# Kernel optimization log

Hardware: AMD Instinct MI355X
Metric: run time of the kernel (lower is better)

Reference implementation:

```python
import jax, jax.numpy as jnp
import numpy as np

N = 4096   # query tokens
M = 4096   # key/value tokens
D = 512    # embedding_dim


def setup_inputs() -> dict:
    key = jax.random.key(0)
    kq, kk, kv = jax.random.split(key, 3)
    return {
        "query": jax.random.normal(kq, (N, D), dtype=jnp.float32),
        "key": jax.random.normal(kk, (M, D), dtype=jnp.float32),
        "value": jax.random.normal(kv, (M, D), dtype=jnp.float32),
    }


def reference(query, key, value):
    # scores = Q K^T  (no 1/sqrt(d) scaling in the original module)
    attention_scores = jnp.einsum("nd,md->nm", query, key)  # [N, M]
    attention_probs = jax.nn.softmax(attention_scores, axis=-1)  # [N, M]
    output = jnp.einsum("nm,md->nd", attention_probs, value)  # [N, D]
    return (output, attention_probs)
```

## Files before the change

kernel.cpp:

```cpp
#include <hip/hip_runtime.h>
#include <hip/hip_bf16.h>
#include <stdint.h>

#define N_Q 4096
#define N_K 4096
#define DIM 512

typedef float f32x4 __attribute__((ext_vector_type(4)));
typedef __bf16 bf16x8 __attribute__((ext_vector_type(8)));
typedef unsigned short u16x4 __attribute__((ext_vector_type(4)));
typedef int i32x4 __attribute__((ext_vector_type(4)));

__device__ __forceinline__ f32x4 mfma_bf16(bf16x8 a, bf16x8 b, f32x4 c) {
  return __builtin_amdgcn_mfma_f32_16x16x32_bf16(a, b, c, 0, 0, 0);
}

__device__ __forceinline__ i32x4 mfma_i8(i32x4 a, i32x4 b, i32x4 c) {
  return __builtin_amdgcn_mfma_i32_16x16x64_i8(a, b, c, 0, 0, 0);
}

__device__ __forceinline__ void gload16(const void* g, void* l) {
  __builtin_amdgcn_global_load_lds((const __attribute__((address_space(1))) void*)g,
                                   (__attribute__((address_space(3))) void*)l,
                                   16, 0, 0);
}

__device__ __forceinline__ void split4(const f32x4 v, u16x4& h, u16x4& l) {
#pragma unroll
  for (int i = 0; i < 4; ++i) {
    float f = v[i];
    uint32_t u = __builtin_bit_cast(uint32_t, f);
    uint32_t hb = (u + 0x8000u) & 0xffff0000u;
    float hf = __builtin_bit_cast(float, hb);
    float lf = f - hf;
    h[i] = (unsigned short)(hb >> 16);
    l[i] = (unsigned short)(__builtin_bit_cast(uint32_t, lf) >> 16);
  }
}

__device__ __forceinline__ unsigned short bf16r(float f) {
  uint32_t u = __builtin_bit_cast(uint32_t, f);
  return (unsigned short)((u + 0x8000u) >> 16);
}

__global__ __launch_bounds__(256) void quant_kernel(const float* __restrict__ Q,
                                                    const float* __restrict__ K,
                                                    signed char* __restrict__ Xq8,
                                                    signed char* __restrict__ Xk8,
                                                    float* __restrict__ sclA,
                                                    float* __restrict__ sclB) {
  const float* X = blockIdx.y ? K : Q;
  signed char* X8 = blockIdx.y ? Xk8 : Xq8;
  float* scl = blockIdx.y ? sclB : sclA;

  const int lane = threadIdx.x & 63;
  const int row = blockIdx.x * 4 + (threadIdx.x >> 6);

  f32x4 v[2];
  v[0] = *(const f32x4*)(X + (size_t)row * DIM + lane * 8);
  v[1] = *(const f32x4*)(X + (size_t)row * DIM + lane * 8 + 4);

  float mx = 0.f;
#pragma unroll
  for (int u = 0; u < 2; ++u)
#pragma unroll
    for (int j = 0; j < 4; ++j) mx = fmaxf(mx, fabsf(v[u][j]));
#pragma unroll
  for (int o = 32; o > 0; o >>= 1) mx = fmaxf(mx, __shfl_xor(mx, o, 64));

  const float s = fmaxf(mx, 1e-20f) * (1.0f / 127.0f);
  const float rinv = 1.0f / s;
  const float linv = 128.0f * rinv;

  uint32_t hw[2], lw[2];
#pragma unroll
  for (int u = 0; u < 2; ++u) {
    uint32_t hword = 0, lword = 0;
#pragma unroll
    for (int j = 0; j < 4; ++j) {
      float x = v[u][j];
      int h = __float2int_rn(x * rinv);
      float r = x - s * (float)h;
      int l = __float2int_rn(r * linv);
      hword |= ((uint32_t)(h & 0xff)) << (8 * j);
      lword |= ((uint32_t)(l & 0xff)) << (8 * j);
    }
    hw[u] = hword; lw[u] = lword;
  }
  uint2 hv; hv.x = hw[0]; hv.y = hw[1];
  uint2 lv; lv.x = lw[0]; lv.y = lw[1];
  *(uint2*)(X8 + (size_t)row * 1024 + lane * 8) = hv;
  *(uint2*)(X8 + (size_t)row * 1024 + 512 + lane * 8) = lv;
  if (lane == 0) scl[row] = s;
}

__global__ __launch_bounds__(256, 2) void qk4_kernel(const signed char* __restrict__ Xq8,
                                                     const signed char* __restrict__ Xk8,
                                                     const float* __restrict__ sclA,
                                                     const float* __restrict__ sclB,
                                                     float* __restrict__ S) {
  __shared__ __align__(16) char smem[65536];

  const int tid = threadIdx.x;
  const int lane = tid & 63, wid = tid >> 6;
  const int wr = wid >> 1, wc = wid & 1;

  const int bid = blockIdx.x;
  const int b = (bid & 7) * 128 + (bid >> 3);
  const int rbase = (b >> 5) * 128;
  const int cbase = (b & 31) * 128;

  const int lrow = lane >> 3;
  const int lchk = lane & 7;

  const i32x4 izero = {0, 0, 0, 0};
  i32x4 acc_hh[4][4], acc_x[4][4];
#pragma unroll
  for (int m = 0; m < 4; ++m)
#pragma unroll
    for (int n = 0; n < 4; ++n) { acc_hh[m][n] = izero; acc_x[m][n] = izero; }

  auto stage = [&](int buf, int t) {
#pragma unroll
    for (int i = 0; i < 4; ++i) {
      const int r = (wid << 5) + (i << 3) + lrow;
      const int sc = lchk ^ (r & 7);
      const int colb = (sc < 4) ? (t * 64 + sc * 16) : (512 + t * 64 + (sc & 3) * 16);
      const signed char* g = Xq8 + (size_t)(rbase + r) * 1024 + colb;
      uint32_t off = (uint32_t)(buf * 32768 + (((wid << 5) + (i << 3)) << 7));
      off = (uint32_t)__builtin_amdgcn_readfirstlane((int)off);
      gload16(g, smem + off);
    }
#pragma unroll
    for (int i = 0; i < 4; ++i) {
      const int r = (wid << 5) + (i << 3) + lrow;
      const int sc = lchk ^ (r & 7);
      const int colb = (sc < 4) ? (t * 64 + sc * 16) : (512 + t * 64 + (sc & 3) * 16);
      const signed char* g = Xk8 + (size_t)(cbase + r) * 1024 + colb;
      uint32_t off = (uint32_t)(buf * 32768 + 16384 + (((wid << 5) + (i << 3)) << 7));
      off = (uint32_t)__builtin_amdgcn_readfirstlane((int)off);
      gload16(g, smem + off);
    }
  };

  auto compute = [&](int buf) {
    const char* bA = smem + buf * 32768;
    const char* bB = bA + 16384;
    const int kc = lane >> 4;
    i32x4 ah[4], al[4], bh[4], bl[4];
#pragma unroll
    for (int m = 0; m < 4; ++m) {
      int row = (wr << 6) + (m << 4) + (lane & 15);
      ah[m] = *(const i32x4*)(bA + row * 128 + ((kc ^ (row & 7)) << 4));
      al[m] = *(const i32x4*)(bA + row * 128 + (((4 + kc) ^ (row & 7)) << 4));
    }
#pragma unroll
    for (int n = 0; n < 4; ++n) {
      int row = (wc << 6) + (n << 4) + (lane & 15);
      bh[n] = *(const i32x4*)(bB + row * 128 + ((kc ^ (row & 7)) << 4));
      bl[n] = *(const i32x4*)(bB + row * 128 + (((4 + kc) ^ (row & 7)) << 4));
    }
    __builtin_amdgcn_s_setprio(1);
#pragma unroll
    for (int m = 0; m < 4; ++m)
#pragma unroll
      for (int n = 0; n < 4; ++n) {
        acc_hh[m][n] = mfma_i8(ah[m], bh[n], acc_hh[m][n]);
        acc_x[m][n]  = mfma_i8(ah[m], bl[n], acc_x[m][n]);
        acc_x[m][n]  = mfma_i8(al[m], bh[n], acc_x[m][n]);
      }
    __builtin_amdgcn_s_setprio(0);
  };

  stage(0, 0);
  stage(1, 1);
  for (int t = 0; t < 8; ++t) {
    if (t < 7) asm volatile("s_waitcnt vmcnt(8)" ::: "memory");
    else       asm volatile("s_waitcnt vmcnt(0)" ::: "memory");
    __builtin_amdgcn_s_barrier();
    compute(t & 1);
    asm volatile("s_waitcnt lgkmcnt(0)" ::: "memory");
    __builtin_amdgcn_sched_barrier(0);
    __builtin_amdgcn_s_barrier();
    if (t + 2 < 8) stage(t & 1, t + 2);
  }

#pragma unroll
  for (int m = 0; m < 4; ++m) {
    int row0 = rbase + wr * 64 + m * 16 + (lane >> 4) * 4;
    float sa[4];
#pragma unroll
    for (int j = 0; j < 4; ++j) sa[j] = sclA[row0 + j];
#pragma unroll
    for (int n = 0; n < 4; ++n) {
      int col = cbase + wc * 64 + n * 16 + (lane & 15);
      float sb = sclB[col];
#pragma unroll
      for (int j = 0; j < 4; ++j) {
        float f = (float)acc_hh[m][n][j] + (float)acc_x[m][n][j] * 0.0078125f;
        S[(size_t)(row0 + j) * N_K + col] = sa[j] * sb * f;
      }
    }
  }
}

__global__ __launch_bounds__(256, 2) void qk_kernel(const float* __restrict__ Q,
                                                    const float* __restrict__ K,
                                                    float* __restrict__ S) {
  __shared__ __align__(16) char sAh[16384];
  __shared__ __align__(16) char sAl[16384];
  __shared__ __align__(16) char sBh[16384];
  __shared__ __align__(16) char sBl[16384];

  const int tid = threadIdx.x;
  const int rbase = blockIdx.y * 128;
  const int cbase = blockIdx.x * 128;
  const int lane = tid & 63, wid = tid >> 6;
  const int wr = wid >> 1, wc = wid & 1;
  const int lr = lane & 15, lk = (lane >> 4) * 8;

  const int srow = tid >> 4;
  const int scol = (tid & 15) * 4;

  f32x4 qr[8], kr[8];
#pragma unroll
  for (int p = 0; p < 8; ++p) {
    int r = p * 16 + srow;
    qr[p] = *(const f32x4*)(Q + (size_t)(rbase + r) * DIM + scol);
    kr[p] = *(const f32x4*)(K + (size_t)(cbase + r) * DIM + scol);
  }

  const f32x4 fzero = {0.f, 0.f, 0.f, 0.f};
  f32x4 acc[4][4];
#pragma unroll
  for (int m = 0; m < 4; ++m)
#pragma unroll
    for (int n = 0; n < 4; ++n) acc[m][n] = fzero;

  for (int kk = 0; kk < DIM / 64; ++kk) {
    __syncthreads();
#pragma unroll
    for (int p = 0; p < 8; ++p) {
      int r = p * 16 + srow;
      uint32_t bo = (uint32_t)(r * 128) + (uint32_t)((scol * 2) ^ ((r & 7) << 4));
      u16x4 qh, ql, kh, kl;
      split4(qr[p], qh, ql);
      split4(kr[p], kh, kl);
      *(u16x4*)(sAh + bo) = qh;
      *(u16x4*)(sAl + bo) = ql;
      *(u16x4*)(sBh + bo) = kh;
      *(u16x4*)(sBl + bo) = kl;
    }
    __syncthreads();
    if (kk < DIM / 64 - 1) {
#pragma unroll
      for (int p = 0; p < 8; ++p) {
        int r = p * 16 + srow;
        qr[p] = *(const f32x4*)(Q + (size_t)(rbase + r) * DIM + (kk + 1) * 64 + scol);
        kr[p] = *(const f32x4*)(K + (size_t)(cbase + r) * DIM + (kk + 1) * 64 + scol);
      }
    }
#pragma unroll
    for (int kh = 0; kh < 2; ++kh) {
      bf16x8 a_h[4], a_l[4], b_h[4], b_l[4];
#pragma unroll
      for (int m = 0; m < 4; ++m) {
        int row = wr * 64 + m * 16 + lr;
        uint32_t co = (uint32_t)(((kh * 32 + lk) * 2) ^ ((row & 7) << 4));
        a_h[m] = *(const bf16x8*)(sAh + row * 128 + co);
        a_l[m] = *(const bf16x8*)(sAl + row * 128 + co);
      }
#pragma unroll
      for (int n = 0; n < 4; ++n) {
        int row = wc * 64 + n * 16 + lr;
        uint32_t co = (uint32_t)(((kh * 32 + lk) * 2) ^ ((row & 7) << 4));
        b_h[n] = *(const bf16x8*)(sBh + row * 128 + co);
        b_l[n] = *(const bf16x8*)(sBl + row * 128 + co);
      }
#pragma unroll
      for (int m = 0; m < 4; ++m)
#pragma unroll
        for (int n = 0; n < 4; ++n) {
          acc[m][n] = mfma_bf16(a_h[m], b_h[n], acc[m][n]);
          acc[m][n] = mfma_bf16(a_h[m], b_l[n], acc[m][n]);
          acc[m][n] = mfma_bf16(a_l[m], b_h[n], acc[m][n]);
        }
    }
  }

#pragma unroll
  for (int m = 0; m < 4; ++m) {
    int row = rbase + wr * 64 + m * 16 + (lane >> 4) * 4;
#pragma unroll
    for (int n = 0; n < 4; ++n) {
      int col = cbase + wc * 64 + n * 16 + lr;
#pragma unroll
      for (int j = 0; j < 4; ++j)
        S[(size_t)(row + j) * N_K + col] = acc[m][n][j];
    }
  }
}

__global__ __launch_bounds__(256) void softmax_kernel(float* __restrict__ P,
                                                      unsigned short* __restrict__ Pb) {
  const int tid = threadIdx.x;
  const int wid = tid >> 6, lane = tid & 63;
  float* p = P + (size_t)blockIdx.x * N_K;

  f32x4 v[4];
  float mx = -3.0e38f;
#pragma unroll
  for (int i = 0; i < 4; ++i) {
    v[i] = *(const f32x4*)(p + i * 1024 + tid * 4);
    mx = fmaxf(mx, fmaxf(fmaxf(v[i][0], v[i][1]), fmaxf(v[i][2], v[i][3])));
  }
#pragma unroll
  for (int o = 32; o > 0; o >>= 1) mx = fmaxf(mx, __shfl_xor(mx, o, 64));
  __shared__ float redM[4];
  __shared__ float redS[4];
  if (lane == 0) redM[wid] = mx;
  __syncthreads();
  mx = fmaxf(fmaxf(redM[0], redM[1]), fmaxf(redM[2], redM[3]));

  float s = 0.f;
#pragma unroll
  for (int i = 0; i < 4; ++i) {
#pragma unroll
    for (int j = 0; j < 4; ++j) {
      v[i][j] = __expf(v[i][j] - mx);
      s += v[i][j];
    }
  }
#pragma unroll
  for (int o = 32; o > 0; o >>= 1) s += __shfl_xor(s, o, 64);
  if (lane == 0) redS[wid] = s;
  __syncthreads();
  s = redS[0] + redS[1] + redS[2] + redS[3];
  const float inv = 1.0f / s;

  unsigned short* pb = Pb ? (Pb + (size_t)blockIdx.x * N_K) : nullptr;
#pragma unroll
  for (int i = 0; i < 4; ++i) {
    v[i] *= inv;
    *(f32x4*)(p + i * 1024 + tid * 4) = v[i];
    if (pb) {
      u16x4 h;
#pragma unroll
      for (int j = 0; j < 4; ++j) h[j] = bf16r(v[i][j]);
      *(u16x4*)(pb + i * 1024 + tid * 4) = h;
    }
  }
}

__global__ __launch_bounds__(256) void vt_kernel(const float* __restrict__ V,
                                                 unsigned short* __restrict__ Vt) {
  __shared__ unsigned short t[64][72];
  const int tid = threadIdx.x;
  const int d0 = blockIdx.x * 64;
  const int k0 = blockIdx.y * 64;

#pragma unroll
  for (int c = 0; c < 4; ++c) {
    int kr = (tid >> 4) + c * 16;
    f32x4 v = *(const f32x4*)(V + (size_t)(k0 + kr) * DIM + d0 + (tid & 15) * 4);
#pragma unroll
    for (int j = 0; j < 4; ++j) t[(tid & 15) * 4 + j][kr] = bf16r(v[j]);
  }
  __syncthreads();
#pragma unroll
  for (int c = 0; c < 2; ++c) {
    int d = (tid >> 3) + c * 32;
    int k = (tid & 7) * 8;
    *(uint4*)(Vt + (size_t)(d0 + d) * N_K + k0 + k) = *(const uint4*)&t[d][k];
  }
}

__global__ __launch_bounds__(256) void zero_kernel(float* __restrict__ O) {
  const f32x4 z = {0.f, 0.f, 0.f, 0.f};
  *(f32x4*)(O + ((size_t)blockIdx.x * 256 + threadIdx.x) * 4) = z;
}

__global__ __launch_bounds__(256, 2) void pv4_kernel(const unsigned short* __restrict__ Pb,
                                                     const unsigned short* __restrict__ Vt,
                                                     float* __restrict__ O) {
  __shared__ __align__(16) char smem[65536];

  const int tid = threadIdx.x;
  const int lane = tid & 63, wid = tid >> 6;
  const int wr = wid >> 1, wc = wid & 1;
  const int rbase = blockIdx.y * 128;
  const int cbase = blockIdx.x * 128;
  const int k0 = blockIdx.z * 1024;

  const int lrow = lane >> 3;
  const int lchk = lane & 7;

  const f32x4 fzero = {0.f, 0.f, 0.f, 0.f};
  f32x4 acc[4][4];
#pragma unroll
  for (int m = 0; m < 4; ++m)
#pragma unroll
    for (int n = 0; n < 4; ++n) acc[m][n] = fzero;

  auto stage = [&](int buf, int t) {
    const size_t kel = (size_t)k0 + ((size_t)t << 6);
#pragma unroll
    for (int i = 0; i < 4; ++i) {
      const int rr = (wid << 5) + (i << 3) + lrow;
      const int gc = lchk ^ (rr & 7);
      const void* gA = (const void*)(Pb + (size_t)(rbase + rr) * N_K + kel + (gc << 3));
      uint32_t off = (uint32_t)(buf * 32768 + (((wid << 5) + (i << 3)) << 7));
      off = (uint32_t)__builtin_amdgcn_readfirstlane((int)off);
      gload16(gA, smem + off);
    }
#pragma unroll
    for (int i = 0; i < 4; ++i) {
      const int rr = (wid << 5) + (i << 3) + lrow;
      const int gc = lchk ^ (rr & 7);
      const void* gB = (const void*)(Vt + (size_t)(cbase + rr) * N_K + kel + (gc << 3));
      uint32_t off = (uint32_t)(buf * 32768 + 16384 + (((wid << 5) + (i << 3)) << 7));
      off = (uint32_t)__builtin_amdgcn_readfirstlane((int)off);
      gload16(gB, smem + off);
    }
  };

  auto compute = [&](int buf) {
    const char* bA = smem + buf * 32768;
    const char* bB = bA + 16384;
#pragma unroll
    for (int kh = 0; kh < 2; ++kh) {
      bf16x8 a[4], bfr[4];
#pragma unroll
      for (int m = 0; m < 4; ++m) {
        int row = (wr << 6) + (m << 4) + (lane & 15);
        uint32_t co = (uint32_t)(((((kh << 2) + (lane >> 4)) << 4)) ^ ((row & 7) << 4));
        a[m] = *(const bf16x8*)(bA + row * 128 + co);
      }
#pragma unroll
      for (int n = 0; n < 4; ++n) {
        int row = (wc << 6) + (n << 4) + (lane & 15);
        uint32_t co = (uint32_t)(((((kh << 2) + (lane >> 4)) << 4)) ^ ((row & 7) << 4));
        bfr[n] = *(const bf16x8*)(bB + row * 128 + co);
      }
      __builtin_amdgcn_s_setprio(1);
#pragma unroll
      for (int m = 0; m < 4; ++m)
#pragma unroll
        for (int n = 0; n < 4; ++n)
          acc[m][n] = mfma_bf16(a[m], bfr[n], acc[m][n]);
      __builtin_amdgcn_s_setprio(0);
    }
  };

  stage(0, 0);
  stage(1, 1);
  for (int t = 0; t < 16; ++t) {
    if (t < 15) asm volatile("s_waitcnt vmcnt(8)" ::: "memory");
    else        asm volatile("s_waitcnt vmcnt(0)" ::: "memory");
    __builtin_amdgcn_s_barrier();
    compute(t & 1);
    asm volatile("s_waitcnt lgkmcnt(0)" ::: "memory");
    __builtin_amdgcn_sched_barrier(0);
    __builtin_amdgcn_s_barrier();
    if (t + 2 < 16) stage(t & 1, t + 2);
  }

#pragma unroll
  for (int m = 0; m < 4; ++m) {
    int row = rbase + wr * 64 + m * 16 + (lane >> 4) * 4;
#pragma unroll
    for (int n = 0; n < 4; ++n) {
      int col = cbase + wc * 64 + n * 16 + (lane & 15);
#pragma unroll
      for (int j = 0; j < 4; ++j)
        atomicAdd(&O[(size_t)(row + j) * DIM + col], acc[m][n][j]);
    }
  }
}

__global__ __launch_bounds__(512, 2) void pv_kernel(const float* __restrict__ P,
                                                    const float* __restrict__ V,
                                                    float* __restrict__ O) {
  __shared__ __align__(16) char sA[16384];
  __shared__ __align__(16) char sB[16384];

  const int tid = threadIdx.x;
  const int rbase = blockIdx.y * 128;
  const int cbase = blockIdx.x * 128;
  const int lane = tid & 63, wid = tid >> 6;
  const int wr = wid >> 2, wc = wid & 3;
  const int lr = lane & 15, lk = (lane >> 4) * 8;

  const int a_row = tid >> 4;
  const int a_col = (tid & 15) * 4;
  const int b_c = tid & 127;
  const int b_oct = tid >> 7;

  f32x4 areg[4];
  float breg[4][4];
#pragma unroll
  for (int p = 0; p < 4; ++p) {
    int r = p * 32 + a_row;
    areg[p] = *(const f32x4*)(P + (size_t)(rbase + r) * N_K + a_col);
  }
#pragma unroll
  for (int g = 0; g < 4; ++g) {
    int kr0 = b_oct * 4 + g * 16;
#pragma unroll
    for (int i = 0; i < 4; ++i)
      breg[g][i] = V[(size_t)(kr0 + i) * DIM + cbase + b_c];
  }

  const f32x4 fzero = {0.f, 0.f, 0.f, 0.f};
  f32x4 acc[4][2];
#pragma unroll
  for (int m = 0; m < 4; ++m)
#pragma unroll
    for (int n = 0; n < 2; ++n) acc[m][n] = fzero;

  for (int kk = 0; kk < N_K / 64; ++kk) {
    __syncthreads();
#pragma unroll
    for (int p = 0; p < 4; ++p) {
      int r = p * 32 + a_row;
      uint32_t bo = (uint32_t)(r * 128) + (uint32_t)((a_col * 2) ^ ((r & 7) << 4));
      u16x4 hv;
#pragma unroll
      for (int i = 0; i < 4; ++i) hv[i] = bf16r(areg[p][i]);
      *(u16x4*)(sA + bo) = hv;
    }
#pragma unroll
    for (int g = 0; g < 4; ++g) {
      int kr0 = b_oct * 4 + g * 16;
      uint32_t bo = (uint32_t)(b_c * 128) + (uint32_t)((kr0 * 2) ^ ((b_c & 7) << 4));
      u16x4 hv;
#pragma unroll
      for (int i = 0; i < 4; ++i) hv[i] = bf16r(breg[g][i]);
      *(u16x4*)(sB + bo) = hv;
    }
    __syncthreads();
    if (kk < N_K / 64 - 1) {
#pragma unroll
      for (int p = 0; p < 4; ++p) {
        int r = p * 32 + a_row;
        areg[p] = *(const f32x4*)(P + (size_t)(rbase + r) * N_K + (kk + 1) * 64 + a_col);
      }
#pragma unroll
      for (int g = 0; g < 4; ++g) {
        int kr0 = b_oct * 4 + g * 16;
#pragma unroll
        for (int i = 0; i < 4; ++i)
          breg[g][i] = V[(size_t)((kk + 1) * 64 + kr0 + i) * DIM + cbase + b_c];
      }
    }
#pragma unroll
    for (int kh = 0; kh < 2; ++kh) {
      bf16x8 af[4], bf[2];
#pragma unroll
      for (int m = 0; m < 4; ++m) {
        int row = wr * 64 + m * 16 + lr;
        uint32_t co = (uint32_t)(((kh * 32 + lk) * 2) ^ ((row & 7) << 4));
        af[m] = *(const bf16x8*)(sA + row * 128 + co);
      }
#pragma unroll
      for (int n = 0; n < 2; ++n) {
        int row = wc * 32 + n * 16 + lr;
        uint32_t co = (uint32_t)(((kh * 32 + lk) * 2) ^ ((row & 7) << 4));
        bf[n] = *(const bf16x8*)(sB + row * 128 + co);
      }
#pragma unroll
      for (int m = 0; m < 4; ++m)
#pragma unroll
        for (int n = 0; n < 2; ++n)
          acc[m][n] = mfma_bf16(af[m], bf[n], acc[m][n]);
    }
  }

#pragma unroll
  for (int m = 0; m < 4; ++m) {
    int row = rbase + wr * 64 + m * 16 + (lane >> 4) * 4;
#pragma unroll
    for (int n = 0; n < 2; ++n) {
      int col = cbase + wc * 32 + n * 16 + lr;
#pragma unroll
      for (int j = 0; j < 4; ++j)
        O[(size_t)(row + j) * DIM + col] = acc[m][n][j];
    }
  }
}

extern "C" void kernel_launch(void* const* d_in, const int* in_sizes, int n_in,
                              void* d_out, int out_size, void* d_ws, size_t ws_size,
                              hipStream_t stream) {
  const float* Q = (const float*)d_in[0];
  const float* K = (const float*)d_in[1];
  const float* V = (const float*)d_in[2];
  float* O = (float*)d_out;
  float* P = O + (size_t)N_Q * DIM;

  const size_t PB_BYTES = (size_t)N_Q * N_K * 2;
  const size_t VT_BYTES = (size_t)DIM * N_K * 2;
  const size_t SCL_BYTES = 65536;

  if (ws_size >= PB_BYTES + VT_BYTES + SCL_BYTES) {
    char* wsb = (char*)d_ws;
    signed char* Xq8 = (signed char*)wsb;
    signed char* Xk8 = Xq8 + (size_t)N_Q * 1024;
    unsigned short* Pb = (unsigned short*)wsb;
    unsigned short* Vt = (unsigned short*)(wsb + PB_BYTES);
    float* sclA = (float*)(wsb + PB_BYTES + VT_BYTES);
    float* sclB = sclA + N_Q;

    quant_kernel<<<dim3(N_Q / 4, 2), 256, 0, stream>>>(Q, K, Xq8, Xk8, sclA, sclB);
    vt_kernel<<<dim3(DIM / 64, N_K / 64), 256, 0, stream>>>(V, Vt);
    qk4_kernel<<<1024, 256, 0, stream>>>(Xq8, Xk8, sclA, sclB, P);
    softmax_kernel<<<N_Q, 256, 0, stream>>>(P, Pb);
    zero_kernel<<<(N_Q * DIM) / (256 * 4), 256, 0, stream>>>(O);
    pv4_kernel<<<dim3(DIM / 128, N_Q / 128, 4), 256, 0, stream>>>(Pb, Vt, O);
  } else {
    qk_kernel<<<dim3(N_K / 128, N_Q / 128), 256, 0, stream>>>(Q, K, P);
    softmax_kernel<<<N_Q, 256, 0, stream>>>(P, nullptr);
    pv_kernel<<<dim3(DIM / 128, N_Q / 128), 512, 0, stream>>>(P, V, O);
  }
}
```

Measured before the change: 129.4 us.

## Merge quant and V-transpose kernels; replace split-K atomics with partial buffers plus reduce

Combines the Q/K int8 quantization and the V bf16 transpose into one prep kernel launch. It also replaces the zero-init plus float atomicAdd split-K accumulation in the PV kernel with plain stores to four partial output buffers, followed by a separate reduction kernel. The goal is to cut launch count and atomic contention. In exchange it adds 32 MB of extra partial-buffer traffic and needs a larger workspace. If the workspace is too small, execution falls back to the slow path.

```diff
diff --git a/kernel.cpp b/kernel.cpp
--- a/kernel.cpp
+++ b/kernel.cpp
@@ -43,55 +43,81 @@
   return (unsigned short)((u + 0x8000u) >> 16);
 }
 
-__global__ __launch_bounds__(256) void quant_kernel(const float* __restrict__ Q,
-                                                    const float* __restrict__ K,
-                                                    signed char* __restrict__ Xq8,
-                                                    signed char* __restrict__ Xk8,
-                                                    float* __restrict__ sclA,
-                                                    float* __restrict__ sclB) {
-  const float* X = blockIdx.y ? K : Q;
-  signed char* X8 = blockIdx.y ? Xk8 : Xq8;
-  float* scl = blockIdx.y ? sclB : sclA;
-
-  const int lane = threadIdx.x & 63;
-  const int row = blockIdx.x * 4 + (threadIdx.x >> 6);
-
-  f32x4 v[2];
-  v[0] = *(const f32x4*)(X + (size_t)row * DIM + lane * 8);
-  v[1] = *(const f32x4*)(X + (size_t)row * DIM + lane * 8 + 4);
-
-  float mx = 0.f;
-#pragma unroll
-  for (int u = 0; u < 2; ++u)
-#pragma unroll
-    for (int j = 0; j < 4; ++j) mx = fmaxf(mx, fabsf(v[u][j]));
-#pragma unroll
-  for (int o = 32; o > 0; o >>= 1) mx = fmaxf(mx, __shfl_xor(mx, o, 64));
-
-  const float s = fmaxf(mx, 1e-20f) * (1.0f / 127.0f);
-  const float rinv = 1.0f / s;
-  const float linv = 128.0f * rinv;
-
-  uint32_t hw[2], lw[2];
-#pragma unroll
-  for (int u = 0; u < 2; ++u) {
-    uint32_t hword = 0, lword = 0;
-#pragma unroll
-    for (int j = 0; j < 4; ++j) {
-      float x = v[u][j];
-      int h = __float2int_rn(x * rinv);
-      float r = x - s * (float)h;
-      int l = __float2int_rn(r * linv);
-      hword |= ((uint32_t)(h & 0xff)) << (8 * j);
-      lword |= ((uint32_t)(l & 0xff)) << (8 * j);
-    }
-    hw[u] = hword; lw[u] = lword;
-  }
-  uint2 hv; hv.x = hw[0]; hv.y = hw[1];
-  uint2 lv; lv.x = lw[0]; lv.y = lw[1];
-  *(uint2*)(X8 + (size_t)row * 1024 + lane * 8) = hv;
-  *(uint2*)(X8 + (size_t)row * 1024 + 512 + lane * 8) = lv;
-  if (lane == 0) scl[row] = s;
+__global__ __launch_bounds__(256) void prep_kernel(const float* __restrict__ Q,
+                                                   const float* __restrict__ K,
+                                                   const float* __restrict__ V,
+                                                   signed char* __restrict__ Xq8,
+                                                   signed char* __restrict__ Xk8,
+                                                   float* __restrict__ sclA,
+                                                   float* __restrict__ sclB,
+                                                   unsigned short* __restrict__ Vt) {
+  __shared__ unsigned short t[64][72];
+  const int bid = blockIdx.x;
+  const int tid = threadIdx.x;
+
+  if (bid < 2048) {
+    const bool isK = bid >= 1024;
+    const float* X = isK ? K : Q;
+    signed char* X8 = isK ? Xk8 : Xq8;
+    float* scl = isK ? sclB : sclA;
+    const int lane = tid & 63;
+    const int row = (isK ? bid - 1024 : bid) * 4 + (tid >> 6);
+
+    f32x4 v[2];
+    v[0] = *(const f32x4*)(X + (size_t)row * DIM + lane * 8);
+    v[1] = *(const f32x4*)(X + (size_t)row * DIM + lane * 8 + 4);
+
+    float mx = 0.f;
+#pragma unroll
+    for (int u = 0; u < 2; ++u)
+#pragma unroll
+      for (int j = 0; j < 4; ++j) mx = fmaxf(mx, fabsf(v[u][j]));
+#pragma unroll
+    for (int o = 32; o > 0; o >>= 1) mx = fmaxf(mx, __shfl_xor(mx, o, 64));
+
+    const float s = fmaxf(mx, 1e-20f) * (1.0f / 127.0f);
+    const float rinv = 1.0f / s;
+    const float linv = 128.0f * rinv;
+
+    uint32_t hw[2], lw[2];
+#pragma unroll
+    for (int u = 0; u < 2; ++u) {
+      uint32_t hword = 0, lword = 0;
+#pragma unroll
+      for (int j = 0; j < 4; ++j) {
+        float x = v[u][j];
+        int h = __float2int_rn(x * rinv);
+        float r = x - s * (float)h;
+        int l = __float2int_rn(r * linv);
+        hword |= ((uint32_t)(h & 0xff)) << (8 * j);
+        lword |= ((uint32_t)(l & 0xff)) << (8 * j);
+      }
+      hw[u] = hword; lw[u] = lword;
+    }
+    uint2 hv; hv.x = hw[0]; hv.y = hw[1];
+    uint2 lv; lv.x = lw[0]; lv.y = lw[1];
+    *(uint2*)(X8 + (size_t)row * 1024 + lane * 8) = hv;
+    *(uint2*)(X8 + (size_t)row * 1024 + 512 + lane * 8) = lv;
+    if (lane == 0) scl[row] = s;
+  } else {
+    const int b2 = bid - 2048;
+    const int d0 = (b2 & 7) * 64;
+    const int k0 = (b2 >> 3) * 64;
+#pragma unroll
+    for (int c = 0; c < 4; ++c) {
+      int kr = (tid >> 4) + c * 16;
+      f32x4 v = *(const f32x4*)(V + (size_t)(k0 + kr) * DIM + d0 + (tid & 15) * 4);
+#pragma unroll
+      for (int j = 0; j < 4; ++j) t[(tid & 15) * 4 + j][kr] = bf16r(v[j]);
+    }
+    __syncthreads();
+#pragma unroll
+    for (int c = 0; c < 2; ++c) {
+      int d = (tid >> 3) + c * 32;
+      int k = (tid & 7) * 8;
+      *(uint4*)(Vt + (size_t)(d0 + d) * N_K + k0 + k) = *(const uint4*)&t[d][k];
+    }
+  }
 }
 
 __global__ __launch_bounds__(256, 2) void qk4_kernel(const signed char* __restrict__ Xq8,
@@ -352,37 +378,9 @@
   }
 }
 
-__global__ __launch_bounds__(256) void vt_kernel(const float* __restrict__ V,
-                                                 unsigned short* __restrict__ Vt) {
-  __shared__ unsigned short t[64][72];
-  const int tid = threadIdx.x;
-  const int d0 = blockIdx.x * 64;
-  const int k0 = blockIdx.y * 64;
-
-#pragma unroll
-  for (int c = 0; c < 4; ++c) {
-    int kr = (tid >> 4) + c * 16;
-    f32x4 v = *(const f32x4*)(V + (size_t)(k0 + kr) * DIM + d0 + (tid & 15) * 4);
-#pragma unroll
-    for (int j = 0; j < 4; ++j) t[(tid & 15) * 4 + j][kr] = bf16r(v[j]);
-  }
-  __syncthreads();
-#pragma unroll
-  for (int c = 0; c < 2; ++c) {
-    int d = (tid >> 3) + c * 32;
-    int k = (tid & 7) * 8;
-    *(uint4*)(Vt + (size_t)(d0 + d) * N_K + k0 + k) = *(const uint4*)&t[d][k];
-  }
-}
-
-__global__ __launch_bounds__(256) void zero_kernel(float* __restrict__ O) {
-  const f32x4 z = {0.f, 0.f, 0.f, 0.f};
-  *(f32x4*)(O + ((size_t)blockIdx.x * 256 + threadIdx.x) * 4) = z;
-}
-
-__global__ __launch_bounds__(256, 2) void pv4_kernel(const unsigned short* __restrict__ Pb,
+__global__ __launch_bounds__(256, 2) void pv5_kernel(const unsigned short* __restrict__ Pb,
                                                      const unsigned short* __restrict__ Vt,
-                                                     float* __restrict__ O) {
+                                                     float* __restrict__ Opart) {
   __shared__ __align__(16) char smem[65536];
 
   const int tid = threadIdx.x;
@@ -391,6 +389,7 @@
   const int rbase = blockIdx.y * 128;
   const int cbase = blockIdx.x * 128;
   const int k0 = blockIdx.z * 1024;
+  float* Out = Opart + (size_t)blockIdx.z * ((size_t)N_Q * DIM);
 
   const int lrow = lane >> 3;
   const int lchk = lane & 7;
@@ -473,9 +472,19 @@
       int col = cbase + wc * 64 + n * 16 + (lane & 15);
 #pragma unroll
       for (int j = 0; j < 4; ++j)
-        atomicAdd(&O[(size_t)(row + j) * DIM + col], acc[m][n][j]);
-    }
-  }
+        Out[(size_t)(row + j) * DIM + col] = acc[m][n][j];
+    }
+  }
+}
+
+__global__ __launch_bounds__(256) void reduce_kernel(float* __restrict__ O,
+                                                     const float* __restrict__ Opart) {
+  size_t i = ((size_t)blockIdx.x * 256 + threadIdx.x) * 4;
+  f32x4 s = *(const f32x4*)(Opart + i);
+#pragma unroll
+  for (int z = 1; z < 4; ++z)
+    s += *(const f32x4*)(Opart + (size_t)z * ((size_t)N_Q * DIM) + i);
+  *(f32x4*)(O + i) = s;
 }
 
 __global__ __launch_bounds__(512, 2) void pv_kernel(const float* __restrict__ P,
@@ -601,8 +610,9 @@
   const size_t PB_BYTES = (size_t)N_Q * N_K * 2;
   const size_t VT_BYTES = (size_t)DIM * N_K * 2;
   const size_t SCL_BYTES = 65536;
-
-  if (ws_size >= PB_BYTES + VT_BYTES + SCL_BYTES) {
+  const size_t OP_BYTES = (size_t)N_Q * DIM * 4;
+
+  if (ws_size >= PB_BYTES + VT_BYTES + SCL_BYTES + 4 * OP_BYTES) {
     char* wsb = (char*)d_ws;
     signed char* Xq8 = (signed char*)wsb;
     signed char* Xk8 = Xq8 + (size_t)N_Q * 1024;
@@ -610,13 +620,13 @@
     unsigned short* Vt = (unsigned short*)(wsb + PB_BYTES);
     float* sclA = (float*)(wsb + PB_BYTES + VT_BYTES);
     float* sclB = sclA + N_Q;
-
-    quant_kernel<<<dim3(N_Q / 4, 2), 256, 0, stream>>>(Q, K, Xq8, Xk8, sclA, sclB);
-    vt_kernel<<<dim3(DIM / 64, N_K / 64), 256, 0, stream>>>(V, Vt);
+    float* Opart = (float*)(wsb + PB_BYTES + VT_BYTES + SCL_BYTES);
+
+    prep_kernel<<<2560, 256, 0, stream>>>(Q, K, V, Xq8, Xk8, sclA, sclB, Vt);
     qk4_kernel<<<1024, 256, 0, stream>>>(Xq8, Xk8, sclA, sclB, P);
     softmax_kernel<<<N_Q, 256, 0, stream>>>(P, Pb);
-    zero_kernel<<<(N_Q * DIM) / (256 * 4), 256, 0, stream>>>(O);
-    pv4_kernel<<<dim3(DIM / 128, N_Q / 128, 4), 256, 0, stream>>>(Pb, Vt, O);
+    pv5_kernel<<<dim3(DIM / 128, N_Q / 128, 4), 256, 0, stream>>>(Pb, Vt, Opart);
+    reduce_kernel<<<(N_Q * DIM) / (256 * 4), 256, 0, stream>>>(O, Opart);
   } else {
     qk_kernel<<<dim3(N_K / 128, N_Q / 128), 256, 0, stream>>>(Q, K, P);
     softmax_kernel<<<N_Q, 256, 0, stream>>>(P, nullptr);
```

New measurement: 114.4 us. -11.6%, faster.
